# Kernel tuning notes

Measured on AMD Instinct MI355X. Metric: run time of the kernel, lower is better.

Reference implementation:

```python
import jax, jax.numpy as jnp
import numpy as np

LMAX, MMAX = 4, 2
C = 128          # sphere_channels
MOUT = 128       # m_output_channels
N = 32768        # number of edges
K = sum(2 * min(l, MMAX) + 1 for l in range(LMAX + 1))  # 19 coefficients
LN_EPS = 1e-5


def build_to_m():
    # l-major ordering of (l, m) coefficients -> m-major permutation matrix
    ms = np.array([m for l in range(LMAX + 1)
                   for m in range(-min(l, MMAX), min(l, MMAX) + 1)])
    order = list(np.nonzero(ms == 0)[0])
    for m in range(1, MMAX + 1):
        order += list(np.nonzero(ms == m)[0]) + list(np.nonzero(ms == -m)[0])
    P = np.zeros((K, K), np.float32)
    P[np.arange(K), order] = 1.0
    return jnp.asarray(P)


TO_M = build_to_m()
M_SIZE = [LMAX + 1] + [LMAX - m + 1 for m in range(1, MMAX + 1)]  # [5, 4, 3]


def _layernorm(h, g, b):
    mu = jnp.mean(h, axis=-1, keepdims=True)
    var = jnp.mean(jnp.square(h - mu), axis=-1, keepdims=True)
    return (h - mu) * jax.lax.rsqrt(var + LN_EPS) * g + b


def _radial_mlp(x, w1, b1, g1, be1, w2, b2, g2, be2, w3, b3):
    h = jax.nn.silu(_layernorm(x @ w1.T + b1, g1, be1))
    h = jax.nn.silu(_layernorm(h @ w2.T + b2, g2, be2))
    return h @ w3.T + b3  # [N, 1536]


def setup_inputs() -> dict:
    key = jax.random.key(0)
    ks = jax.random.split(key, 16)
    s = 0.02
    return {
        "x": jax.random.normal(ks[0], (N, K, C), jnp.float32),
        "x_edge": jax.random.normal(ks[1], (N, C), jnp.float32),
        "fc0_w": jax.random.normal(ks[2], (MOUT * 5, 5 * C), jnp.float32) * s,
        "fc0_b": jax.random.normal(ks[3], (MOUT * 5,), jnp.float32) * s,
        "fc1_w": jax.random.normal(ks[4], (MOUT * 4, 4 * C), jnp.float32) * s,
        "fc2_w": jax.random.normal(ks[5], (MOUT * 3, 3 * C), jnp.float32) * s,
        "rad_w1": jax.random.normal(ks[6], (C, C), jnp.float32) * s,
        "rad_b1": jax.random.normal(ks[7], (C,), jnp.float32) * s,
        "rad_g1": jnp.ones((C,), jnp.float32),
        "rad_beta1": jnp.zeros((C,), jnp.float32),
        "rad_w2": jax.random.normal(ks[8], (C, C), jnp.float32) * s,
        "rad_b2": jax.random.normal(ks[9], (C,), jnp.float32) * s,
        "rad_g2": jnp.ones((C,), jnp.float32),
        "rad_beta2": jnp.zeros((C,), jnp.float32),
        "rad_w3": jax.random.normal(ks[10], (1536, C), jnp.float32) * s,
        "rad_b3": jax.random.normal(ks[11], (1536,), jnp.float32) * s,
    }


def reference(x, x_edge, fc0_w, fc0_b, fc1_w, fc2_w,
              rad_w1, rad_b1, rad_g1, rad_beta1,
              rad_w2, rad_b2, rad_g2, rad_beta2,
              rad_w3, rad_b3):
    n = x.shape[0]
    # reorder coefficients by m (to_m is a permutation)
    xm = jnp.einsum('nac,ba->nbc', x, TO_M)
    rad = _radial_mlp(x_edge, rad_w1, rad_b1, rad_g1, rad_beta1,
                      rad_w2, rad_b2, rad_g2, rad_beta2, rad_w3, rad_b3)

    # m = 0 block
    sz0 = M_SIZE[0]
    x0 = xm[:, :sz0].reshape(n, sz0 * C) * rad[:, :sz0 * C]
    y0 = (x0 @ fc0_w.T + fc0_b).reshape(n, sz0, MOUT)
    outs = [y0]

    offset, offr = sz0, sz0 * C
    for m, fcw in zip((1, 2), (fc1_w, fc2_w)):
        sz = M_SIZE[m]
        din = sz * C
        xb = xm[:, offset:offset + 2 * sz].reshape(n, 2, din)
        xb = xb * rad[:, offr:offr + din][:, None, :]  # FiLM radial scale
        yb = (xb @ fcw.T).reshape(n, 2 * sz, MOUT)
        outs.append(yb)
        offset += 2 * sz
        offr += din

    out = jnp.concatenate(outs, axis=1)  # [N, K, MOUT]
    # project back from m-major ordering
    return jnp.einsum('nac,ab->nbc', out, TO_M)
```

## Files before the change

### kernel.cpp

```cpp
#include <hip/hip_runtime.h>

typedef __bf16 bf16x8 __attribute__((ext_vector_type(8)));
typedef __bf16 bf16x4 __attribute__((ext_vector_type(4)));
typedef float f32x4 __attribute__((ext_vector_type(4)));

#define MFMA_16x16x32_BF16(a, b, c) __builtin_amdgcn_mfma_f32_16x16x32_bf16(a, b, c, 0, 0, 0)

typedef const __attribute__((address_space(1))) unsigned int* gas_ptr;
typedef __attribute__((address_space(3))) unsigned int* las_ptr;

__device__ __forceinline__ void gload_lds16(const void* g, void* l) {
    __builtin_amdgcn_global_load_lds((gas_ptr)(unsigned long long)g,
                                     (las_ptr)(unsigned long long)l, 16, 0, 0);
}

__constant__ int ORDER_C[19] = {0, 2, 6, 11, 16, 3, 7, 12, 17, 1, 5, 10, 15, 8, 13, 18, 4, 9, 14};

__global__ __launch_bounds__(256) void wxconv_kernel(
    const float* __restrict__ fc0, const float* __restrict__ fc1,
    const float* __restrict__ fc2, const float* __restrict__ rw1,
    const float* __restrict__ rw2, const float* __restrict__ rw3,
    const float* __restrict__ xe, __bf16* __restrict__ wo,
    __bf16* __restrict__ xo) {
    const int bid = blockIdx.x;
    const float* s;
    __bf16* o;
    int i4, rel;
    if (bid < 1024) {
        i4 = (bid * 256 + threadIdx.x) * 4;
        o = wo;
        if (i4 < 409600)      { s = fc0; rel = i4; }
        else if (i4 < 671744) { s = fc1; rel = i4 - 409600; }
        else if (i4 < 819200) { s = fc2; rel = i4 - 671744; }
        else if (i4 < 835584) { s = rw1; rel = i4 - 819200; }
        else if (i4 < 851968) { s = rw2; rel = i4 - 835584; }
        else                  { s = rw3; rel = i4 - 851968; }
    } else {
        i4 = ((bid - 1024) * 256 + threadIdx.x) * 4;
        o = xo; s = xe; rel = i4;
    }
    float4 v = *(const float4*)(s + rel);
    bf16x4 b;
    b[0] = (__bf16)v.x; b[1] = (__bf16)v.y; b[2] = (__bf16)v.z; b[3] = (__bf16)v.w;
    *(bf16x4*)(o + i4) = b;
}

__global__ __launch_bounds__(256) void gemmln_kernel(
    const __bf16* __restrict__ Ain, const __bf16* __restrict__ Wb,
    const float* __restrict__ bvec, const float* __restrict__ gv,
    const float* __restrict__ bev, __bf16* __restrict__ hs) {
    __shared__ __align__(16) char smem[49152];
    __bf16* As = (__bf16*)smem;
    __bf16* Bs = (__bf16*)(smem + 16384);
    float*  Fs = (float*)smem;
    const int tid = threadIdx.x;
    const int w = tid >> 6, lane = tid & 63;
    const int quad = lane >> 4, l16 = lane & 15;
    const int e0 = blockIdx.x * 64;

    {
        const char* ga = (const char*)(Ain + (size_t)e0 * 128);
        const char* gb = (const char*)Wb;
        for (int r = 0; r < 4; ++r) {
            int boff = (r * 4 + w) * 1024 + lane * 16;
            int soff = boff ^ (((boff >> 8) & 15) << 4);
            gload_lds16(ga + soff, (char*)As + boff);
        }
        for (int r = 0; r < 8; ++r) {
            int boff = (r * 4 + w) * 1024 + lane * 16;
            int soff = boff ^ (((boff >> 8) & 15) << 4);
            gload_lds16(gb + soff, (char*)Bs + boff);
        }
    }
    __syncthreads();

    const int wr = w >> 1, wc = w & 1;
    f32x4 acc[2][4] = {};
    for (int ks = 0; ks < 4; ++ks) {
        bf16x8 af[2], bfr[4];
        for (int i = 0; i < 2; ++i) {
            int ar = wr * 32 + i * 16 + l16;
            af[i] = *(const bf16x8*)&As[ar * 128 + ((ks * 32 + quad * 8) ^ ((ar & 15) << 3))];
        }
        for (int j = 0; j < 4; ++j) {
            int br = wc * 64 + j * 16 + l16;
            bfr[j] = *(const bf16x8*)&Bs[br * 128 + ((ks * 32 + quad * 8) ^ ((br & 15) << 3))];
        }
        for (int i = 0; i < 2; ++i)
            for (int j = 0; j < 4; ++j)
                acc[i][j] = MFMA_16x16x32_BF16(af[i], bfr[j], acc[i][j]);
    }
    __syncthreads();

    float bc[4];
    for (int j = 0; j < 4; ++j) bc[j] = bvec[wc * 64 + j * 16 + l16];
    for (int i = 0; i < 2; ++i)
        for (int j = 0; j < 4; ++j)
            for (int r = 0; r < 4; ++r)
                Fs[(wr * 32 + i * 16 + quad * 4 + r) * 128 + wc * 64 + j * 16 + l16] =
                    acc[i][j][r] + bc[j];
    __syncthreads();

    const float gl = gv[lane], gh = gv[lane + 64];
    const float bl = bev[lane], bh = bev[lane + 64];
    for (int it = 0; it < 16; ++it) {
        const int row = it * 4 + w;
        float a = Fs[row * 128 + lane];
        float b = Fs[row * 128 + lane + 64];
        float s = a + b;
        s += __shfl_xor(s, 1);  s += __shfl_xor(s, 2);  s += __shfl_xor(s, 4);
        s += __shfl_xor(s, 8);  s += __shfl_xor(s, 16); s += __shfl_xor(s, 32);
        const float mu = s * (1.f / 128.f);
        const float da = a - mu, db = b - mu;
        float v = da * da + db * db;
        v += __shfl_xor(v, 1);  v += __shfl_xor(v, 2);  v += __shfl_xor(v, 4);
        v += __shfl_xor(v, 8);  v += __shfl_xor(v, 16); v += __shfl_xor(v, 32);
        const float rs = rsqrtf(v * (1.f / 128.f) + 1e-5f);
        float ya = da * rs * gl + bl;
        float yb = db * rs * gh + bh;
        ya = ya / (1.f + __expf(-ya));
        yb = yb / (1.f + __expf(-yb));
        hs[(size_t)(e0 + row) * 128 + lane] = (__bf16)ya;
        hs[(size_t)(e0 + row) * 128 + lane + 64] = (__bf16)yb;
    }
}

__global__ __launch_bounds__(256) void radial3_film_kernel(
    const __bf16* __restrict__ h2g, const __bf16* __restrict__ w3b,
    const float* __restrict__ b3, const float* __restrict__ xg,
    __bf16* __restrict__ Aws) {
    __shared__ __align__(16) __bf16 As[128 * 128];
    __shared__ __align__(16) __bf16 Bs[128 * 128];
    const int tid = threadIdx.x;
    const int w = tid >> 6, lane = tid & 63;
    const int quad = lane >> 4, l16 = lane & 15;
    const int y = blockIdx.y;
    const int e0 = blockIdx.x * 128, n0 = y * 128;

    {
        const char* ga = (const char*)(h2g + (size_t)e0 * 128);
        const char* gb = (const char*)(w3b + (size_t)n0 * 128);
        for (int r = 0; r < 8; ++r) {
            int boff = (r * 4 + w) * 1024 + lane * 16;
            int soff = boff ^ (((boff >> 8) & 15) << 4);
            gload_lds16(ga + soff, (char*)As + boff);
            gload_lds16(gb + soff, (char*)Bs + boff);
        }
    }
    __syncthreads();

    const int wr = w >> 1, wc = w & 1;
    f32x4 acc[4][4] = {};
    for (int ks = 0; ks < 4; ++ks) {
        bf16x8 af[4], bfr[4];
        for (int i = 0; i < 4; ++i) {
            int ar = wr * 64 + i * 16 + l16;
            af[i] = *(const bf16x8*)&As[ar * 128 + ((ks * 32 + quad * 8) ^ ((ar & 15) << 3))];
        }
        for (int j = 0; j < 4; ++j) {
            int br = wc * 64 + j * 16 + l16;
            bfr[j] = *(const bf16x8*)&Bs[br * 128 + ((ks * 32 + quad * 8) ^ ((br & 15) << 3))];
        }
        for (int i = 0; i < 4; ++i)
            for (int j = 0; j < 4; ++j)
                acc[i][j] = MFMA_16x16x32_BF16(af[i], bfr[j], acc[i][j]);
    }
    __syncthreads();

    float bcol[4];
    for (int j = 0; j < 4; ++j) bcol[j] = b3[n0 + wc * 64 + j * 16 + l16];
    for (int i = 0; i < 4; ++i)
        for (int j = 0; j < 4; ++j)
            for (int r = 0; r < 4; ++r) {
                int row = wr * 64 + i * 16 + quad * 4 + r;
                int col = wc * 64 + j * 16 + l16;
                As[row * 128 + col] = (__bf16)(acc[i][j][r] + bcol[j]);
            }
    __syncthreads();

    int nb, bs0, bs1;
    if (y < 5)      { nb = 1; bs0 = y;     bs1 = 0; }
    else if (y < 9) { nb = 2; bs0 = y;     bs1 = y + 4; }
    else            { nb = 2; bs0 = y + 4; bs1 = y + 7; }

    for (int t = 0; t < nb; ++t) {
        const int b = t ? bs1 : bs0;
        const int xrow = ORDER_C[b];
        for (int r = 0; r < 8; ++r) {
            int idx = r * 256 + tid;
            int e = idx >> 4, c = (idx & 15) * 8;
            bf16x8 rv = *(const bf16x8*)&As[e * 128 + c];
            const float* xp = xg + (size_t)(e0 + e) * 2432 + xrow * 128 + c;
            float4 x0 = *(const float4*)xp;
            float4 x1 = *(const float4*)(xp + 4);
            bf16x8 av;
            av[0] = (__bf16)(x0.x * (float)rv[0]);
            av[1] = (__bf16)(x0.y * (float)rv[1]);
            av[2] = (__bf16)(x0.z * (float)rv[2]);
            av[3] = (__bf16)(x0.w * (float)rv[3]);
            av[4] = (__bf16)(x1.x * (float)rv[4]);
            av[5] = (__bf16)(x1.y * (float)rv[5]);
            av[6] = (__bf16)(x1.z * (float)rv[6]);
            av[7] = (__bf16)(x1.w * (float)rv[7]);
            *(bf16x8*)(Aws + (size_t)(e0 + e) * 2432 + b * 128 + c) = av;
        }
    }
}

__global__ __launch_bounds__(256, 2) void so2_gemm_kernel(
    const __bf16* __restrict__ Aws, const __bf16* __restrict__ wfc0,
    const __bf16* __restrict__ wfc1, const __bf16* __restrict__ wfc2,
    const float* __restrict__ fc0b, float* __restrict__ outg) {
    __shared__ __align__(16) char smem[65536];
    const int tid = threadIdx.x;
    const int w = tid >> 6, lane = tid & 63;
    const int quad = lane >> 4, l16 = lane & 15;

    const int bid = blockIdx.x;
    const int wg = (bid & 7) * 608 + (bid >> 3);
    const int y = wg % 19;
    const int e0 = (wg / 19) * 128;

    int bstart, sz;
    const __bf16* W;
    if (y < 5)       { bstart = 0;  sz = 5; W = wfc0; }
    else if (y < 9)  { bstart = 5;  sz = 4; W = wfc1; }
    else if (y < 13) { bstart = 9;  sz = 4; W = wfc1; }
    else if (y < 16) { bstart = 13; sz = 3; W = wfc2; }
    else             { bstart = 16; sz = 3; W = wfc2; }
    const int K = sz * 128, s_out = y - bstart, nkt = 2 * sz;
    const char* abase = (const char*)Aws + (size_t)bstart * 256;
    const char* wbase = (const char*)W + (size_t)s_out * 128 * K * 2;

#define STAGE(buf, kt)                                                              \
    {                                                                               \
        const char* ak = abase + (size_t)(kt) * 128;                                \
        const char* wk = wbase + (size_t)(kt) * 128;                                \
        char* la = smem + (buf) * 16384;                                            \
        char* lb = smem + 32768 + (buf) * 16384;                                    \
        for (int r = 0; r < 4; ++r) {                                               \
            int boff = (r * 4 + w) * 1024 + lane * 16;                              \
            int row = boff >> 7, kb = boff & 127;                                   \
            int skb = kb ^ ((row & 7) << 4);                                        \
            gload_lds16(ak + (size_t)(e0 + row) * 4864 + skb, la + boff);           \
            gload_lds16(wk + (size_t)row * (size_t)(K * 2) + skb, lb + boff);       \
        }                                                                           \
    }

    const int wr = w >> 1, wc = w & 1;
    f32x4 acc[4][4] = {};
    STAGE(0, 0);
    for (int kt = 0; kt < nkt; ++kt) {
        const int cur = kt & 1;
        if (kt + 1 < nkt) {
            STAGE(cur ^ 1, kt + 1);
            asm volatile("s_waitcnt vmcnt(8)" ::: "memory");
        } else {
            asm volatile("s_waitcnt vmcnt(0)" ::: "memory");
        }
        __builtin_amdgcn_s_barrier();

        const __bf16* Asc = (const __bf16*)(smem + cur * 16384);
        const __bf16* Bsc = (const __bf16*)(smem + 32768 + cur * 16384);
        bf16x8 af[2][4], bfr[2][4];
        for (int ks = 0; ks < 2; ++ks) {
            for (int i = 0; i < 4; ++i) {
                int ar = wr * 64 + i * 16 + l16;
                af[ks][i] = *(const bf16x8*)&Asc[ar * 64 + ((ks * 32 + quad * 8) ^ ((ar & 7) << 3))];
            }
            for (int j = 0; j < 4; ++j) {
                int br = wc * 64 + j * 16 + l16;
                bfr[ks][j] = *(const bf16x8*)&Bsc[br * 64 + ((ks * 32 + quad * 8) ^ ((br & 7) << 3))];
            }
        }
        asm volatile("s_waitcnt lgkmcnt(0)" ::: "memory");
        __builtin_amdgcn_s_barrier();

        __builtin_amdgcn_s_setprio(1);
        for (int ks = 0; ks < 2; ++ks)
            for (int i = 0; i < 4; ++i)
                for (int j = 0; j < 4; ++j)
                    acc[i][j] = MFMA_16x16x32_BF16(af[ks][i], bfr[ks][j], acc[i][j]);
        __builtin_amdgcn_s_setprio(0);
    }
#undef STAGE

    const int outrow = ORDER_C[y];
    float bv[4];
    for (int j = 0; j < 4; ++j)
        bv[j] = (y < 5) ? fc0b[s_out * 128 + wc * 64 + j * 16 + l16] : 0.f;
    float* Fs = (float*)smem;
    for (int i = 0; i < 4; ++i)
        for (int j = 0; j < 4; ++j)
            for (int r = 0; r < 4; ++r)
                Fs[(wr * 64 + i * 16 + quad * 4 + r) * 128 + wc * 64 + j * 16 + l16] =
                    acc[i][j][r] + bv[j];
    __syncthreads();
    for (int t = 0; t < 16; ++t) {
        int idx = t * 256 + tid;
        int row = idx >> 5, c4 = (idx & 31) * 4;
        *(float4*)(outg + (size_t)(e0 + row) * 2432 + outrow * 128 + c4) =
            *(const float4*)&Fs[row * 128 + c4];
    }
}

extern "C" void kernel_launch(void* const* d_in, const int* in_sizes, int n_in,
                              void* d_out, int out_size, void* d_ws, size_t ws_size,
                              hipStream_t stream) {
    const float* x       = (const float*)d_in[0];
    const float* x_edge  = (const float*)d_in[1];
    const float* fc0_w   = (const float*)d_in[2];
    const float* fc0_b   = (const float*)d_in[3];
    const float* fc1_w   = (const float*)d_in[4];
    const float* fc2_w   = (const float*)d_in[5];
    const float* rad_w1  = (const float*)d_in[6];
    const float* rad_b1  = (const float*)d_in[7];
    const float* rad_g1  = (const float*)d_in[8];
    const float* rad_be1 = (const float*)d_in[9];
    const float* rad_w2  = (const float*)d_in[10];
    const float* rad_b2  = (const float*)d_in[11];
    const float* rad_g2  = (const float*)d_in[12];
    const float* rad_be2 = (const float*)d_in[13];
    const float* rad_w3  = (const float*)d_in[14];
    const float* rad_b3  = (const float*)d_in[15];
    float* out = (float*)d_out;

    const int N = in_sizes[0] / (19 * 128);

    __bf16* wb  = (__bf16*)d_ws;
    __bf16* sh  = (__bf16*)((char*)d_ws + (2u << 20));
    __bf16* Aws = (__bf16*)((char*)d_ws + (10u << 20));
    __bf16* h1  = Aws;
    __bf16* wfc0 = wb;
    __bf16* wfc1 = wb + 409600;
    __bf16* wfc2 = wb + 671744;
    __bf16* w1b  = wb + 819200;
    __bf16* w2b  = wb + 835584;
    __bf16* w3b  = wb + 851968;

    wxconv_kernel<<<dim3(5120), dim3(256), 0, stream>>>(fc0_w, fc1_w, fc2_w, rad_w1,
                                                        rad_w2, rad_w3, x_edge, wb, sh);
    gemmln_kernel<<<dim3(N / 64), dim3(256), 0, stream>>>(sh, w1b, rad_b1, rad_g1,
                                                          rad_be1, h1);
    gemmln_kernel<<<dim3(N / 64), dim3(256), 0, stream>>>(h1, w2b, rad_b2, rad_g2,
                                                          rad_be2, sh);
    radial3_film_kernel<<<dim3(N / 128, 12), dim3(256), 0, stream>>>(sh, w3b, rad_b3,
                                                                     x, Aws);
    so2_gemm_kernel<<<dim3(8 * 608), dim3(256), 0, stream>>>(Aws, wfc0, wfc1, wfc2,
                                                             fc0_b, out);
}
```

Measured before the change: 725.1 us.

## Fuse radial MLP layers and enlarge SO2 GEMM tiles with triple buffering

Merges the two gemm+layernorm+silu kernels into one radial12 kernel that keeps the first hidden activation in LDS, so it no longer round-trips through global memory. This also saves one launch. The SO(2) GEMM moves to 512-thread blocks with a 256-edge tile and a three-stage global-to-LDS pipeline, and writes its epilogue in two halves. The larger tiles are meant to reuse each weight tile across more edges and hide load latency, at the cost of 144KB of LDS and one block per CU.

```diff
diff --git a/kernel.cpp b/kernel.cpp
--- a/kernel.cpp
+++ b/kernel.cpp
@@ -45,22 +45,26 @@
     *(bf16x4*)(o + i4) = b;
 }
 
-__global__ __launch_bounds__(256) void gemmln_kernel(
-    const __bf16* __restrict__ Ain, const __bf16* __restrict__ Wb,
-    const float* __restrict__ bvec, const float* __restrict__ gv,
-    const float* __restrict__ bev, __bf16* __restrict__ hs) {
-    __shared__ __align__(16) char smem[49152];
+__global__ __launch_bounds__(256) void radial12_kernel(
+    const __bf16* __restrict__ xeb, const __bf16* __restrict__ w1b,
+    const __bf16* __restrict__ w2b,
+    const float* __restrict__ b1, const float* __restrict__ g1,
+    const float* __restrict__ be1,
+    const float* __restrict__ b2, const float* __restrict__ g2,
+    const float* __restrict__ be2, __bf16* __restrict__ h2out) {
+    __shared__ __align__(16) char smem[81920];
     __bf16* As = (__bf16*)smem;
     __bf16* Bs = (__bf16*)(smem + 16384);
-    float*  Fs = (float*)smem;
+    float*  Fs = (float*)(smem + 49152);
     const int tid = threadIdx.x;
     const int w = tid >> 6, lane = tid & 63;
     const int quad = lane >> 4, l16 = lane & 15;
     const int e0 = blockIdx.x * 64;
-
-    {
-        const char* ga = (const char*)(Ain + (size_t)e0 * 128);
-        const char* gb = (const char*)Wb;
+    const int wr = w >> 1, wc = w & 1;
+
+    {
+        const char* ga = (const char*)(xeb + (size_t)e0 * 128);
+        const char* gb = (const char*)w1b;
         for (int r = 0; r < 4; ++r) {
             int boff = (r * 4 + w) * 1024 + lane * 16;
             int soff = boff ^ (((boff >> 8) & 15) << 4);
@@ -74,7 +78,6 @@
     }
     __syncthreads();
 
-    const int wr = w >> 1, wc = w & 1;
     f32x4 acc[2][4] = {};
     for (int ks = 0; ks < 4; ++ks) {
         bf16x8 af[2], bfr[4];
@@ -92,36 +95,102 @@
     }
     __syncthreads();
 
-    float bc[4];
-    for (int j = 0; j < 4; ++j) bc[j] = bvec[wc * 64 + j * 16 + l16];
-    for (int i = 0; i < 2; ++i)
-        for (int j = 0; j < 4; ++j)
-            for (int r = 0; r < 4; ++r)
-                Fs[(wr * 32 + i * 16 + quad * 4 + r) * 128 + wc * 64 + j * 16 + l16] =
-                    acc[i][j][r] + bc[j];
-    __syncthreads();
-
-    const float gl = gv[lane], gh = gv[lane + 64];
-    const float bl = bev[lane], bh = bev[lane + 64];
-    for (int it = 0; it < 16; ++it) {
-        const int row = it * 4 + w;
-        float a = Fs[row * 128 + lane];
-        float b = Fs[row * 128 + lane + 64];
-        float s = a + b;
-        s += __shfl_xor(s, 1);  s += __shfl_xor(s, 2);  s += __shfl_xor(s, 4);
-        s += __shfl_xor(s, 8);  s += __shfl_xor(s, 16); s += __shfl_xor(s, 32);
-        const float mu = s * (1.f / 128.f);
-        const float da = a - mu, db = b - mu;
-        float v = da * da + db * db;
-        v += __shfl_xor(v, 1);  v += __shfl_xor(v, 2);  v += __shfl_xor(v, 4);
-        v += __shfl_xor(v, 8);  v += __shfl_xor(v, 16); v += __shfl_xor(v, 32);
-        const float rs = rsqrtf(v * (1.f / 128.f) + 1e-5f);
-        float ya = da * rs * gl + bl;
-        float yb = db * rs * gh + bh;
-        ya = ya / (1.f + __expf(-ya));
-        yb = yb / (1.f + __expf(-yb));
-        hs[(size_t)(e0 + row) * 128 + lane] = (__bf16)ya;
-        hs[(size_t)(e0 + row) * 128 + lane + 64] = (__bf16)yb;
+    {
+        const char* gb = (const char*)w2b;
+        for (int r = 0; r < 8; ++r) {
+            int boff = (r * 4 + w) * 1024 + lane * 16;
+            int soff = boff ^ (((boff >> 8) & 15) << 4);
+            gload_lds16(gb + soff, (char*)Bs + boff);
+        }
+    }
+
+    {
+        float bc[4];
+        for (int j = 0; j < 4; ++j) bc[j] = b1[wc * 64 + j * 16 + l16];
+        for (int i = 0; i < 2; ++i)
+            for (int j = 0; j < 4; ++j)
+                for (int r = 0; r < 4; ++r)
+                    Fs[(wr * 32 + i * 16 + quad * 4 + r) * 128 + wc * 64 + j * 16 + l16] =
+                        acc[i][j][r] + bc[j];
+    }
+    __syncthreads();
+
+    {
+        const float gl = g1[lane], gh = g1[lane + 64];
+        const float bl = be1[lane], bh = be1[lane + 64];
+        for (int it = 0; it < 16; ++it) {
+            const int row = it * 4 + w;
+            float a = Fs[row * 128 + lane];
+            float b = Fs[row * 128 + lane + 64];
+            float s = a + b;
+            s += __shfl_xor(s, 1);  s += __shfl_xor(s, 2);  s += __shfl_xor(s, 4);
+            s += __shfl_xor(s, 8);  s += __shfl_xor(s, 16); s += __shfl_xor(s, 32);
+            const float mu = s * (1.f / 128.f);
+            const float da = a - mu, db = b - mu;
+            float v = da * da + db * db;
+            v += __shfl_xor(v, 1);  v += __shfl_xor(v, 2);  v += __shfl_xor(v, 4);
+            v += __shfl_xor(v, 8);  v += __shfl_xor(v, 16); v += __shfl_xor(v, 32);
+            const float rs = rsqrtf(v * (1.f / 128.f) + 1e-5f);
+            float ya = da * rs * gl + bl;
+            float yb = db * rs * gh + bh;
+            ya = ya / (1.f + __expf(-ya));
+            yb = yb / (1.f + __expf(-yb));
+            As[row * 128 + (lane ^ ((row & 15) << 3))] = (__bf16)ya;
+            As[row * 128 + ((lane + 64) ^ ((row & 15) << 3))] = (__bf16)yb;
+        }
+    }
+    __syncthreads();
+
+    f32x4 acc2[2][4] = {};
+    for (int ks = 0; ks < 4; ++ks) {
+        bf16x8 af[2], bfr[4];
+        for (int i = 0; i < 2; ++i) {
+            int ar = wr * 32 + i * 16 + l16;
+            af[i] = *(const bf16x8*)&As[ar * 128 + ((ks * 32 + quad * 8) ^ ((ar & 15) << 3))];
+        }
+        for (int j = 0; j < 4; ++j) {
+            int br = wc * 64 + j * 16 + l16;
+            bfr[j] = *(const bf16x8*)&Bs[br * 128 + ((ks * 32 + quad * 8) ^ ((br & 15) << 3))];
+        }
+        for (int i = 0; i < 2; ++i)
+            for (int j = 0; j < 4; ++j)
+                acc2[i][j] = MFMA_16x16x32_BF16(af[i], bfr[j], acc2[i][j]);
+    }
+
+    {
+        float bc[4];
+        for (int j = 0; j < 4; ++j) bc[j] = b2[wc * 64 + j * 16 + l16];
+        for (int i = 0; i < 2; ++i)
+            for (int j = 0; j < 4; ++j)
+                for (int r = 0; r < 4; ++r)
+                    Fs[(wr * 32 + i * 16 + quad * 4 + r) * 128 + wc * 64 + j * 16 + l16] =
+                        acc2[i][j][r] + bc[j];
+    }
+    __syncthreads();
+
+    {
+        const float gl = g2[lane], gh = g2[lane + 64];
+        const float bl = be2[lane], bh = be2[lane + 64];
+        for (int it = 0; it < 16; ++it) {
+            const int row = it * 4 + w;
+            float a = Fs[row * 128 + lane];
+            float b = Fs[row * 128 + lane + 64];
+            float s = a + b;
+            s += __shfl_xor(s, 1);  s += __shfl_xor(s, 2);  s += __shfl_xor(s, 4);
+            s += __shfl_xor(s, 8);  s += __shfl_xor(s, 16); s += __shfl_xor(s, 32);
+            const float mu = s * (1.f / 128.f);
+            const float da = a - mu, db = b - mu;
+            float v = da * da + db * db;
+            v += __shfl_xor(v, 1);  v += __shfl_xor(v, 2);  v += __shfl_xor(v, 4);
+            v += __shfl_xor(v, 8);  v += __shfl_xor(v, 16); v += __shfl_xor(v, 32);
+            const float rs = rsqrtf(v * (1.f / 128.f) + 1e-5f);
+            float ya = da * rs * gl + bl;
+            float yb = db * rs * gh + bh;
+            ya = ya / (1.f + __expf(-ya));
+            yb = yb / (1.f + __expf(-yb));
+            h2out[(size_t)(e0 + row) * 128 + lane] = (__bf16)ya;
+            h2out[(size_t)(e0 + row) * 128 + lane + 64] = (__bf16)yb;
+        }
     }
 }
 
@@ -207,19 +276,19 @@
     }
 }
 
-__global__ __launch_bounds__(256, 2) void so2_gemm_kernel(
+__global__ __launch_bounds__(512, 1) void so2_gemm_kernel(
     const __bf16* __restrict__ Aws, const __bf16* __restrict__ wfc0,
     const __bf16* __restrict__ wfc1, const __bf16* __restrict__ wfc2,
     const float* __restrict__ fc0b, float* __restrict__ outg) {
-    __shared__ __align__(16) char smem[65536];
+    __shared__ __align__(16) char smem[147456];
     const int tid = threadIdx.x;
     const int w = tid >> 6, lane = tid & 63;
     const int quad = lane >> 4, l16 = lane & 15;
 
     const int bid = blockIdx.x;
-    const int wg = (bid & 7) * 608 + (bid >> 3);
+    const int wg = (bid & 7) * 304 + (bid >> 3);
     const int y = wg % 19;
-    const int e0 = (wg / 19) * 128;
+    const int e0 = (wg / 19) * 256;
 
     int bstart, sz;
     const __bf16* W;
@@ -236,13 +305,18 @@
     {                                                                               \
         const char* ak = abase + (size_t)(kt) * 128;                                \
         const char* wk = wbase + (size_t)(kt) * 128;                                \
-        char* la = smem + (buf) * 16384;                                            \
-        char* lb = smem + 32768 + (buf) * 16384;                                    \
+        char* la = smem + (buf) * 32768;                                            \
+        char* lb = smem + 98304 + (buf) * 16384;                                    \
         for (int r = 0; r < 4; ++r) {                                               \
-            int boff = (r * 4 + w) * 1024 + lane * 16;                              \
+            int boff = (r * 8 + w) * 1024 + lane * 16;                              \
             int row = boff >> 7, kb = boff & 127;                                   \
             int skb = kb ^ ((row & 7) << 4);                                        \
             gload_lds16(ak + (size_t)(e0 + row) * 4864 + skb, la + boff);           \
+        }                                                                           \
+        for (int r = 0; r < 2; ++r) {                                               \
+            int boff = (r * 8 + w) * 1024 + lane * 16;                              \
+            int row = boff >> 7, kb = boff & 127;                                   \
+            int skb = kb ^ ((row & 7) << 4);                                        \
             gload_lds16(wk + (size_t)row * (size_t)(K * 2) + skb, lb + boff);       \
         }                                                                           \
     }
@@ -250,18 +324,22 @@
     const int wr = w >> 1, wc = w & 1;
     f32x4 acc[4][4] = {};
     STAGE(0, 0);
+    STAGE(1, 1);
+    int cur = 0;
     for (int kt = 0; kt < nkt; ++kt) {
-        const int cur = kt & 1;
-        if (kt + 1 < nkt) {
-            STAGE(cur ^ 1, kt + 1);
-            asm volatile("s_waitcnt vmcnt(8)" ::: "memory");
+        if (kt + 2 < nkt) {
+            const int nb = (cur == 0) ? 2 : (cur == 1 ? 0 : 1);
+            STAGE(nb, kt + 2);
+            asm volatile("s_waitcnt vmcnt(12)" ::: "memory");
+        } else if (kt + 1 < nkt) {
+            asm volatile("s_waitcnt vmcnt(6)" ::: "memory");
         } else {
             asm volatile("s_waitcnt vmcnt(0)" ::: "memory");
         }
         __builtin_amdgcn_s_barrier();
 
-        const __bf16* Asc = (const __bf16*)(smem + cur * 16384);
-        const __bf16* Bsc = (const __bf16*)(smem + 32768 + cur * 16384);
+        const __bf16* Asc = (const __bf16*)(smem + cur * 32768);
+        const __bf16* Bsc = (const __bf16*)(smem + 98304 + cur * 16384);
         bf16x8 af[2][4], bfr[2][4];
         for (int ks = 0; ks < 2; ++ks) {
             for (int i = 0; i < 4; ++i) {
@@ -282,6 +360,7 @@
                 for (int j = 0; j < 4; ++j)
                     acc[i][j] = MFMA_16x16x32_BF16(af[ks][i], bfr[ks][j], acc[i][j]);
         __builtin_amdgcn_s_setprio(0);
+        cur = (cur == 2) ? 0 : cur + 1;
     }
 #undef STAGE
 
@@ -290,17 +369,22 @@
     for (int j = 0; j < 4; ++j)
         bv[j] = (y < 5) ? fc0b[s_out * 128 + wc * 64 + j * 16 + l16] : 0.f;
     float* Fs = (float*)smem;
-    for (int i = 0; i < 4; ++i)
-        for (int j = 0; j < 4; ++j)
-            for (int r = 0; r < 4; ++r)
-                Fs[(wr * 64 + i * 16 + quad * 4 + r) * 128 + wc * 64 + j * 16 + l16] =
-                    acc[i][j][r] + bv[j];
-    __syncthreads();
-    for (int t = 0; t < 16; ++t) {
-        int idx = t * 256 + tid;
-        int row = idx >> 5, c4 = (idx & 31) * 4;
-        *(float4*)(outg + (size_t)(e0 + row) * 2432 + outrow * 128 + c4) =
-            *(const float4*)&Fs[row * 128 + c4];
+    for (int p = 0; p < 2; ++p) {
+        if ((wr >> 1) == p) {
+            for (int i = 0; i < 4; ++i)
+                for (int j = 0; j < 4; ++j)
+                    for (int r = 0; r < 4; ++r)
+                        Fs[((wr & 1) * 64 + i * 16 + quad * 4 + r) * 128 + wc * 64 + j * 16 + l16] =
+                            acc[i][j][r] + bv[j];
+        }
+        __syncthreads();
+        for (int t = 0; t < 8; ++t) {
+            int idx = t * 512 + tid;
+            int row = idx >> 5, c4 = (idx & 31) * 4;
+            *(float4*)(outg + (size_t)(e0 + p * 128 + row) * 2432 + outrow * 128 + c4) =
+                *(const float4*)&Fs[row * 128 + c4];
+        }
+        if (p == 0) __syncthreads();
     }
 }
 
@@ -328,9 +412,9 @@
     const int N = in_sizes[0] / (19 * 128);
 
     __bf16* wb  = (__bf16*)d_ws;
-    __bf16* sh  = (__bf16*)((char*)d_ws + (2u << 20));
-    __bf16* Aws = (__bf16*)((char*)d_ws + (10u << 20));
-    __bf16* h1  = Aws;
+    __bf16* xeb = (__bf16*)((char*)d_ws + (2u << 20));
+    __bf16* h2  = (__bf16*)((char*)d_ws + (10u << 20));
+    __bf16* Aws = (__bf16*)((char*)d_ws + (18u << 20));
     __bf16* wfc0 = wb;
     __bf16* wfc1 = wb + 409600;
     __bf16* wfc2 = wb + 671744;
@@ -339,13 +423,11 @@
     __bf16* w3b  = wb + 851968;
 
     wxconv_kernel<<<dim3(5120), dim3(256), 0, stream>>>(fc0_w, fc1_w, fc2_w, rad_w1,
-                                                        rad_w2, rad_w3, x_edge, wb, sh);
-    gemmln_kernel<<<dim3(N / 64), dim3(256), 0, stream>>>(sh, w1b, rad_b1, rad_g1,
-                                                          rad_be1, h1);
-    gemmln_kernel<<<dim3(N / 64), dim3(256), 0, stream>>>(h1, w2b, rad_b2, rad_g2,
-                                                          rad_be2, sh);
-    radial3_film_kernel<<<dim3(N / 128, 12), dim3(256), 0, stream>>>(sh, w3b, rad_b3,
+                                                        rad_w2, rad_w3, x_edge, wb, xeb);
+    radial12_kernel<<<dim3(N / 64), dim3(256), 0, stream>>>(
+        xeb, w1b, w2b, rad_b1, rad_g1, rad_be1, rad_b2, rad_g2, rad_be2, h2);
+    radial3_film_kernel<<<dim3(N / 128, 12), dim3(256), 0, stream>>>(h2, w3b, rad_b3,
                                                                      x, Aws);
-    so2_gemm_kernel<<<dim3(8 * 608), dim3(256), 0, stream>>>(Aws, wfc0, wfc1, wfc2,
-                                                             fc0_b, out);
-}
+    so2_gemm_kernel<<<dim3(2432), dim3(512), 0, stream>>>(Aws, wfc0, wfc1, wfc2,
+                                                          fc0_b, out);
+}
```

New measurement: 722.1 us. Within noise of the previous version (-0.4%).
